# Optimization experiments

Hardware: AMD Instinct MI355X
Metric: run time of the kernel (lower is better)

## Reference

```python
import jax, jax.numpy as jnp
import numpy as np

B, N, DK, DV = 16, 4096, 64, 64


def setup_inputs() -> dict:
    key = jax.random.key(0)
    kq, kk, kv = jax.random.split(key, 3)
    q = jax.random.normal(kq, (B, N, DK), dtype=jnp.float32)
    k = jax.random.normal(kk, (B, N, DK), dtype=jnp.float32)
    v = jax.random.normal(kv, (B, N, DV), dtype=jnp.float32)
    # causal mask: positions j<=i are attendable (mask==True)
    mask = jnp.tril(jnp.ones((N, N), dtype=bool))[None, :, :]  # (1, N, N)
    return {"q": q, "k": k, "v": v, "mask": mask}


def reference(q, k, v, mask):
    # scores: (B, N, N)
    scale = 1.0 / jnp.sqrt(jnp.asarray(q.shape[-1], dtype=q.dtype))
    scores = jnp.einsum('bnd,bmd->bnm', q, k) * scale
    scores = jnp.where(mask, scores, jnp.asarray(-jnp.inf, dtype=scores.dtype))
    attn = jax.nn.softmax(scores, axis=-1)
    # dropout is identity in eval/reference mode
    return jnp.einsum('bnm,bmd->bnd', attn, v)
```

## Files before the change

### kernel.cpp

```cpp
#include <hip/hip_runtime.h>


#define N_SEQ 4096
#define DIM   64

typedef __bf16  bf16x8 __attribute__((ext_vector_type(8)));
typedef unsigned short u16x8 __attribute__((ext_vector_type(8)));
typedef float   f32x4  __attribute__((ext_vector_type(4)));
typedef short   short4v __attribute__((ext_vector_type(4)));

static __device__ __forceinline__ unsigned short f2bf(float f) {
    unsigned int u = __float_as_uint(f);
    u += 0x7FFFu + ((u >> 16) & 1u);
    return (unsigned short)(u >> 16);
}

static __device__ __forceinline__ unsigned int pk2bf(float a, float b) {
#if defined(__HIP_DEVICE_COMPILE__) && __has_builtin(__builtin_amdgcn_cvt_pk_bf16_f32)
    typedef __bf16 bf16x2_t __attribute__((ext_vector_type(2)));
    bf16x2_t r = __builtin_amdgcn_cvt_pk_bf16_f32(a, b);
    return __builtin_bit_cast(unsigned int, r);
#else
    return (unsigned int)f2bf(a) | ((unsigned int)f2bf(b) << 16);
#endif
}

static __device__ __forceinline__ float fexp2(float x) {
#if defined(__HIP_DEVICE_COMPILE__) && __has_builtin(__builtin_amdgcn_exp2f)
    return __builtin_amdgcn_exp2f(x);
#else
    return exp2f(x);
#endif
}

static __device__ __forceinline__ bf16x8 ld_frag(const void* p) {
    u16x8 u = *reinterpret_cast<const u16x8*>(p);
    return __builtin_bit_cast(bf16x8, u);
}

static __device__ __forceinline__ f32x4 mfma_pv(uint2 a, uint2 b, f32x4 c) {
#if defined(__HIP_DEVICE_COMPILE__)
#if __has_builtin(__builtin_amdgcn_mfma_f32_16x16x16bf16_1k)
    return __builtin_amdgcn_mfma_f32_16x16x16bf16_1k(
        __builtin_bit_cast(short4v, a), __builtin_bit_cast(short4v, b), c, 0, 0, 0);
#else
    f32x4 d;
    asm volatile("v_mfma_f32_16x16x16_bf16 %0, %1, %2, %3"
                 : "=v"(d) : "v"(a), "v"(b), "v"(c));
    return d;
#endif
#else
    (void)a; (void)b;
    return c;
#endif
}

static __device__ __forceinline__ void gl_lds16(const unsigned short* g, unsigned short* l) {
#if defined(__HIP_DEVICE_COMPILE__)
    __builtin_amdgcn_global_load_lds(
        (const __attribute__((address_space(1))) unsigned int*)(g),
        (__attribute__((address_space(3))) unsigned int*)(l), 16, 0, 0);
#else
    (void)g; (void)l;
#endif
}

__global__ __launch_bounds__(256)
void prep_kv(const float* __restrict__ K, const float* __restrict__ V,
             unsigned short* __restrict__ wsK, unsigned short* __restrict__ wsV) {
    const int b = blockIdx.y, t = blockIdx.x;
    if (blockIdx.z == 0) {
        const float* src = K + ((size_t)b * N_SEQ + t * 64) * DIM;
        unsigned short* dst = wsK + ((size_t)(b * 64 + t)) * 4096;
        #pragma unroll
        for (int ph = 0; ph < 2; ++ph) {
            const int gidx = threadIdx.x + ph * 256;
            const int r = gidx >> 3, g = gidx & 7;
            const float* p = src + r * DIM + g * 8;
            f32x4 f0 = *reinterpret_cast<const f32x4*>(p);
            f32x4 f1 = *reinterpret_cast<const f32x4*>(p + 4);
            uint4 w;
            w.x = pk2bf(f0[0], f0[1]); w.y = pk2bf(f0[2], f0[3]);
            w.z = pk2bf(f1[0], f1[1]); w.w = pk2bf(f1[2], f1[3]);
            *reinterpret_cast<uint4*>(&dst[(r * 8 + (g ^ (r & 7))) * 8]) = w;
        }
    } else {
        const int dv = threadIdx.x & 63;
        const int g0 = threadIdx.x >> 6;
        const float* src = V + ((size_t)b * N_SEQ + t * 64) * DIM + dv;
        unsigned short* dst = wsV + ((size_t)(b * 64 + t)) * 4096;
        #pragma unroll
        for (int ph = 0; ph < 2; ++ph) {
            const int g = g0 + ph * 4;
            float p[8];
            #pragma unroll
            for (int i = 0; i < 8; ++i)
                p[i] = src[(size_t)(g * 8 + i) * DIM];
            uint4 w;
            w.x = pk2bf(p[0], p[1]); w.y = pk2bf(p[2], p[3]);
            w.z = pk2bf(p[4], p[5]); w.w = pk2bf(p[6], p[7]);
            *reinterpret_cast<uint4*>(&dst[(dv * 8 + (g ^ (dv & 7))) * 8]) = w;
        }
    }
}

__global__ __launch_bounds__(256)
void attn_fwd(const float* __restrict__ Q, const unsigned short* __restrict__ wsK,
              const unsigned short* __restrict__ wsV, float* __restrict__ O) {
    __shared__ unsigned short kbuf[2][4096];
    __shared__ unsigned short vbuf[2][4096];

    const int tid  = threadIdx.x;
    const int wave = tid >> 6;
    const int lane = tid & 63;
    const int quad = lane >> 4;
    const int ln   = lane & 15;
    const int ln7  = lane & 7;

    const int L = (int)blockIdx.x;
    const int u = L & 255, v = L >> 8;
    const int p_ = u + ((v >> 1) << 8);
    const int b    = p_ >> 5;
    const int j    = p_ & 31;
    const int tile = (v & 1) ? (63 - j) : j;
    const int i0   = tile * 64;
    const int tmax = tile;

    const float QS = 0.125f * 1.44269504f;
    const int qrow = i0 + wave * 16 + ln;
    const float* qptr = Q + ((size_t)b * N_SEQ + qrow) * DIM;
    u16x8 qa[2];
    #pragma unroll
    for (int s = 0; s < 2; ++s) {
        const float* p = qptr + s * 32 + quad * 8;
        f32x4 f0 = *reinterpret_cast<const f32x4*>(p);
        f32x4 f1 = *reinterpret_cast<const f32x4*>(p + 4);
        #pragma unroll
        for (int jj = 0; jj < 4; ++jj) {
            qa[s][jj]     = f2bf(f0[jj] * QS);
            qa[s][4 + jj] = f2bf(f1[jj] * QS);
        }
    }

    int kaddr[8];
    #pragma unroll
    for (int s = 0; s < 2; ++s)
        #pragma unroll
        for (int nt = 0; nt < 4; ++nt)
            kaddr[s * 4 + nt] = (nt * 16 + ln) * 128 + (((s * 4 + quad) ^ ln7) * 16);
    int vaddr[16];
    #pragma unroll
    for (int nt = 0; nt < 4; ++nt)
        #pragma unroll
        for (int dvt = 0; dvt < 4; ++dvt)
            vaddr[nt * 4 + dvt] = (dvt * 16 + ln) * 128
                                + (((nt * 2 + (quad >> 1)) ^ ln7) * 16) + (quad & 1) * 8;

    const unsigned short* kt_src = wsK + (size_t)b * 64 * 4096;
    const unsigned short* vt_src = wsV + (size_t)b * 64 * 4096;
    const int dma_off = wave * 1024 + lane * 8;

    auto dma = [&](int t, int bufi) {
        const unsigned short* ks = kt_src + (size_t)t * 4096 + dma_off;
        const unsigned short* vs = vt_src + (size_t)t * 4096 + dma_off;
        #pragma unroll
        for (int i = 0; i < 2; ++i) {
            gl_lds16(ks + i * 512, &kbuf[bufi][wave * 1024 + i * 512]);
            gl_lds16(vs + i * 512, &vbuf[bufi][wave * 1024 + i * 512]);
        }
    };

    f32x4 o_acc[4] = {};
    float lsum = 0.f;

    auto compute = [&](int t, const unsigned short* kb, const unsigned short* vb) {
        f32x4 st[4] = {};
        #pragma unroll
        for (int s = 0; s < 2; ++s) {
            bf16x8 qf = __builtin_bit_cast(bf16x8, qa[s]);
            #pragma unroll
            for (int nt = 0; nt < 4; ++nt) {
                bf16x8 kf = ld_frag((const char*)kb + kaddr[s * 4 + nt]);
                st[nt] = __builtin_amdgcn_mfma_f32_16x16x32_bf16(kf, qf, st[nt], 0, 0, 0);
            }
        }
        uint2 bvv[16];
        #pragma unroll
        for (int i = 0; i < 16; ++i)
            bvv[i] = *reinterpret_cast<const uint2*>((const char*)vb + vaddr[i]);

        uint2 pk_d[4];
        if (t == tmax) {
            const int qloc = wave * 16 + ln;
            #pragma unroll
            for (int nt = 0; nt < 4; ++nt) {
                float p[4];
                #pragma unroll
                for (int r = 0; r < 4; ++r) {
                    const int kp = nt * 16 + quad * 4 + r;
                    const float x = (kp > qloc) ? -3.0e38f : st[nt][r];
                    p[r] = fexp2(x);
                    lsum += p[r];
                }
                pk_d[nt].x = pk2bf(p[0], p[1]);
                pk_d[nt].y = pk2bf(p[2], p[3]);
            }
        } else {
            #pragma unroll
            for (int nt = 0; nt < 4; ++nt) {
                float p[4];
                #pragma unroll
                for (int r = 0; r < 4; ++r) {
                    p[r] = fexp2(st[nt][r]);
                    lsum += p[r];
                }
                pk_d[nt].x = pk2bf(p[0], p[1]);
                pk_d[nt].y = pk2bf(p[2], p[3]);
            }
        }
        #pragma unroll
        for (int nt = 0; nt < 4; ++nt)
            #pragma unroll
            for (int dvt = 0; dvt < 4; ++dvt)
                o_acc[dvt] = mfma_pv(pk_d[nt], bvv[nt * 4 + dvt], o_acc[dvt]);
    };

    dma(0, 0);
    int t = 0;
    while (true) {
        __syncthreads();
        if (t < tmax) dma(t + 1, 1);
        compute(t, kbuf[0], vbuf[0]);
        if (t == tmax) break;
        ++t;
        __syncthreads();
        if (t < tmax) dma(t + 1, 0);
        compute(t, kbuf[1], vbuf[1]);
        if (t == tmax) break;
        ++t;
    }

    float s = lsum;
    s += __shfl_xor(s, 16, 64);
    s += __shfl_xor(s, 32, 64);
    float linv[4];
    #pragma unroll
    for (int r = 0; r < 4; ++r)
        linv[r] = 1.0f / __shfl(s, quad * 4 + r, 64);

    float* obase = O + ((size_t)b * N_SEQ + i0 + wave * 16) * DIM;
    #pragma unroll
    for (int r = 0; r < 4; ++r)
        #pragma unroll
        for (int dvt = 0; dvt < 4; ++dvt)
            obase[(quad * 4 + r) * DIM + dvt * 16 + ln] = o_acc[dvt][r] * linv[r];
}

extern "C" void kernel_launch(void* const* d_in, const int* in_sizes, int n_in,
                              void* d_out, int out_size, void* d_ws, size_t ws_size,
                              hipStream_t stream) {
    const float* q = (const float*)d_in[0];
    const float* k = (const float*)d_in[1];
    const float* v = (const float*)d_in[2];
    float* out = (float*)d_out;

    unsigned short* wsK = (unsigned short*)d_ws;
    unsigned short* wsV = wsK + (size_t)16 * 64 * 4096;

    prep_kv<<<dim3(64, 16, 2), dim3(256), 0, stream>>>(k, v, wsK, wsV);
    attn_fwd<<<dim3(1024), dim3(256), 0, stream>>>(q, wsK, wsV, out);
}
```

Measured before the change: 212.3 us.

## Use persistent blocks with atomic work queue and MFMA row-sum

Replaces the static 1024-block causal tile mapping with 512 persistent blocks that pull query tiles, longest first, from per-XCD atomic counters. The counters are reset in prep_kv. The goal is better load balance across the uneven causal workloads. The softmax denominator is now accumulated by an extra MFMA against a vector of ones, replacing per-lane scalar sums and shuffles. This adds an atomic plus two barriers per work item, and relies on blockIdx&7 mapping to an XCD for locality.

```diff
diff --git a/kernel.cpp b/kernel.cpp
--- a/kernel.cpp
+++ b/kernel.cpp
@@ -8,6 +8,8 @@
 typedef unsigned short u16x8 __attribute__((ext_vector_type(8)));
 typedef float   f32x4  __attribute__((ext_vector_type(4)));
 typedef short   short4v __attribute__((ext_vector_type(4)));
+
+__device__ int g_qcount[8];
 
 static __device__ __forceinline__ unsigned short f2bf(float f) {
     unsigned int u = __float_as_uint(f);
@@ -68,6 +70,8 @@
 __global__ __launch_bounds__(256)
 void prep_kv(const float* __restrict__ K, const float* __restrict__ V,
              unsigned short* __restrict__ wsK, unsigned short* __restrict__ wsV) {
+    if (blockIdx.x == 0 && blockIdx.y == 0 && blockIdx.z == 0 && threadIdx.x < 8)
+        g_qcount[threadIdx.x] = 0;
     const int b = blockIdx.y, t = blockIdx.x;
     if (blockIdx.z == 0) {
         const float* src = K + ((size_t)b * N_SEQ + t * 64) * DIM;
@@ -109,6 +113,7 @@
               const unsigned short* __restrict__ wsV, float* __restrict__ O) {
     __shared__ unsigned short kbuf[2][4096];
     __shared__ unsigned short vbuf[2][4096];
+    __shared__ int s_item;
 
     const int tid  = threadIdx.x;
     const int wave = tid >> 6;
@@ -116,31 +121,7 @@
     const int quad = lane >> 4;
     const int ln   = lane & 15;
     const int ln7  = lane & 7;
-
-    const int L = (int)blockIdx.x;
-    const int u = L & 255, v = L >> 8;
-    const int p_ = u + ((v >> 1) << 8);
-    const int b    = p_ >> 5;
-    const int j    = p_ & 31;
-    const int tile = (v & 1) ? (63 - j) : j;
-    const int i0   = tile * 64;
-    const int tmax = tile;
-
-    const float QS = 0.125f * 1.44269504f;
-    const int qrow = i0 + wave * 16 + ln;
-    const float* qptr = Q + ((size_t)b * N_SEQ + qrow) * DIM;
-    u16x8 qa[2];
-    #pragma unroll
-    for (int s = 0; s < 2; ++s) {
-        const float* p = qptr + s * 32 + quad * 8;
-        f32x4 f0 = *reinterpret_cast<const f32x4*>(p);
-        f32x4 f1 = *reinterpret_cast<const f32x4*>(p + 4);
-        #pragma unroll
-        for (int jj = 0; jj < 4; ++jj) {
-            qa[s][jj]     = f2bf(f0[jj] * QS);
-            qa[s][4 + jj] = f2bf(f1[jj] * QS);
-        }
-    }
+    const int r    = (int)blockIdx.x & 7;
 
     int kaddr[8];
     #pragma unroll
@@ -156,104 +137,120 @@
             vaddr[nt * 4 + dvt] = (dvt * 16 + ln) * 128
                                 + (((nt * 2 + (quad >> 1)) ^ ln7) * 16) + (quad & 1) * 8;
 
-    const unsigned short* kt_src = wsK + (size_t)b * 64 * 4096;
-    const unsigned short* vt_src = wsV + (size_t)b * 64 * 4096;
     const int dma_off = wave * 1024 + lane * 8;
-
-    auto dma = [&](int t, int bufi) {
-        const unsigned short* ks = kt_src + (size_t)t * 4096 + dma_off;
-        const unsigned short* vs = vt_src + (size_t)t * 4096 + dma_off;
-        #pragma unroll
-        for (int i = 0; i < 2; ++i) {
-            gl_lds16(ks + i * 512, &kbuf[bufi][wave * 1024 + i * 512]);
-            gl_lds16(vs + i * 512, &vbuf[bufi][wave * 1024 + i * 512]);
-        }
-    };
-
-    f32x4 o_acc[4] = {};
-    float lsum = 0.f;
-
-    auto compute = [&](int t, const unsigned short* kb, const unsigned short* vb) {
-        f32x4 st[4] = {};
+    const uint2 ones  = make_uint2(0x3F803F80u, 0x3F803F80u);
+    const float QS = 0.125f * 1.44269504f;
+
+    for (;;) {
+        __syncthreads();
+        if (tid == 0) s_item = atomicAdd(&g_qcount[r], 1);
+        __syncthreads();
+        const int item = s_item;
+        if (item >= 128) break;
+
+        const int tile = 63 - (item >> 1);
+        const int b    = r * 2 + (item & 1);
+        const int i0   = tile * 64;
+        const int tmax = tile;
+
+        const float* qptr = Q + ((size_t)b * N_SEQ + i0 + wave * 16 + ln) * DIM;
+        u16x8 qa[2];
         #pragma unroll
         for (int s = 0; s < 2; ++s) {
-            bf16x8 qf = __builtin_bit_cast(bf16x8, qa[s]);
+            const float* p = qptr + s * 32 + quad * 8;
+            f32x4 f0 = *reinterpret_cast<const f32x4*>(p);
+            f32x4 f1 = *reinterpret_cast<const f32x4*>(p + 4);
+            #pragma unroll
+            for (int jj = 0; jj < 4; ++jj) {
+                qa[s][jj]     = f2bf(f0[jj] * QS);
+                qa[s][4 + jj] = f2bf(f1[jj] * QS);
+            }
+        }
+
+        const unsigned short* kt_src = wsK + (size_t)b * 64 * 4096;
+        const unsigned short* vt_src = wsV + (size_t)b * 64 * 4096;
+
+        auto dma = [&](int t, int bufi) {
+            const unsigned short* ks = kt_src + (size_t)t * 4096 + dma_off;
+            const unsigned short* vs = vt_src + (size_t)t * 4096 + dma_off;
+            #pragma unroll
+            for (int i = 0; i < 2; ++i) {
+                gl_lds16(ks + i * 512, &kbuf[bufi][wave * 1024 + i * 512]);
+                gl_lds16(vs + i * 512, &vbuf[bufi][wave * 1024 + i * 512]);
+            }
+        };
+
+        f32x4 o_acc[4] = {};
+        f32x4 lacc = {};
+
+        auto compute = [&](int t, const unsigned short* kb, const unsigned short* vb) {
+            f32x4 st[4] = {};
+            #pragma unroll
+            for (int s = 0; s < 2; ++s) {
+                bf16x8 qf = __builtin_bit_cast(bf16x8, qa[s]);
+                #pragma unroll
+                for (int nt = 0; nt < 4; ++nt) {
+                    bf16x8 kf = ld_frag((const char*)kb + kaddr[s * 4 + nt]);
+                    st[nt] = __builtin_amdgcn_mfma_f32_16x16x32_bf16(kf, qf, st[nt], 0, 0, 0);
+                }
+            }
+            uint2 bvv[16];
+            #pragma unroll
+            for (int i = 0; i < 16; ++i)
+                bvv[i] = *reinterpret_cast<const uint2*>((const char*)vb + vaddr[i]);
+
+            uint2 pk_d[4];
+            if (t == tmax) {
+                const int qloc = wave * 16 + ln;
+                #pragma unroll
+                for (int nt = 0; nt < 4; ++nt) {
+                    float p0 = fexp2((nt * 16 + quad * 4 + 0 > qloc) ? -3.0e38f : st[nt][0]);
+                    float p1 = fexp2((nt * 16 + quad * 4 + 1 > qloc) ? -3.0e38f : st[nt][1]);
+                    float p2 = fexp2((nt * 16 + quad * 4 + 2 > qloc) ? -3.0e38f : st[nt][2]);
+                    float p3 = fexp2((nt * 16 + quad * 4 + 3 > qloc) ? -3.0e38f : st[nt][3]);
+                    pk_d[nt].x = pk2bf(p0, p1);
+                    pk_d[nt].y = pk2bf(p2, p3);
+                }
+            } else {
+                #pragma unroll
+                for (int nt = 0; nt < 4; ++nt) {
+                    pk_d[nt].x = pk2bf(fexp2(st[nt][0]), fexp2(st[nt][1]));
+                    pk_d[nt].y = pk2bf(fexp2(st[nt][2]), fexp2(st[nt][3]));
+                }
+            }
             #pragma unroll
             for (int nt = 0; nt < 4; ++nt) {
-                bf16x8 kf = ld_frag((const char*)kb + kaddr[s * 4 + nt]);
-                st[nt] = __builtin_amdgcn_mfma_f32_16x16x32_bf16(kf, qf, st[nt], 0, 0, 0);
-            }
-        }
-        uint2 bvv[16];
-        #pragma unroll
-        for (int i = 0; i < 16; ++i)
-            bvv[i] = *reinterpret_cast<const uint2*>((const char*)vb + vaddr[i]);
-
-        uint2 pk_d[4];
-        if (t == tmax) {
-            const int qloc = wave * 16 + ln;
-            #pragma unroll
-            for (int nt = 0; nt < 4; ++nt) {
-                float p[4];
-                #pragma unroll
-                for (int r = 0; r < 4; ++r) {
-                    const int kp = nt * 16 + quad * 4 + r;
-                    const float x = (kp > qloc) ? -3.0e38f : st[nt][r];
-                    p[r] = fexp2(x);
-                    lsum += p[r];
-                }
-                pk_d[nt].x = pk2bf(p[0], p[1]);
-                pk_d[nt].y = pk2bf(p[2], p[3]);
-            }
-        } else {
-            #pragma unroll
-            for (int nt = 0; nt < 4; ++nt) {
-                float p[4];
-                #pragma unroll
-                for (int r = 0; r < 4; ++r) {
-                    p[r] = fexp2(st[nt][r]);
-                    lsum += p[r];
-                }
-                pk_d[nt].x = pk2bf(p[0], p[1]);
-                pk_d[nt].y = pk2bf(p[2], p[3]);
-            }
-        }
-        #pragma unroll
-        for (int nt = 0; nt < 4; ++nt)
+                #pragma unroll
+                for (int dvt = 0; dvt < 4; ++dvt)
+                    o_acc[dvt] = mfma_pv(pk_d[nt], bvv[nt * 4 + dvt], o_acc[dvt]);
+                lacc = mfma_pv(pk_d[nt], ones, lacc);
+            }
+        };
+
+        dma(0, 0);
+        int t = 0;
+        while (true) {
+            __syncthreads();
+            if (t < tmax) dma(t + 1, 1);
+            compute(t, kbuf[0], vbuf[0]);
+            if (t == tmax) break;
+            ++t;
+            __syncthreads();
+            if (t < tmax) dma(t + 1, 0);
+            compute(t, kbuf[1], vbuf[1]);
+            if (t == tmax) break;
+            ++t;
+        }
+
+        float* obase = O + ((size_t)b * N_SEQ + i0 + wave * 16) * DIM;
+        #pragma unroll
+        for (int rr = 0; rr < 4; ++rr) {
+            const float inv = 1.0f / lacc[rr];
             #pragma unroll
             for (int dvt = 0; dvt < 4; ++dvt)
-                o_acc[dvt] = mfma_pv(pk_d[nt], bvv[nt * 4 + dvt], o_acc[dvt]);
-    };
-
-    dma(0, 0);
-    int t = 0;
-    while (true) {
-        __syncthreads();
-        if (t < tmax) dma(t + 1, 1);
-        compute(t, kbuf[0], vbuf[0]);
-        if (t == tmax) break;
-        ++t;
-        __syncthreads();
-        if (t < tmax) dma(t + 1, 0);
-        compute(t, kbuf[1], vbuf[1]);
-        if (t == tmax) break;
-        ++t;
+                obase[(quad * 4 + rr) * DIM + dvt * 16 + ln] = o_acc[dvt][rr] * inv;
+        }
     }
-
-    float s = lsum;
-    s += __shfl_xor(s, 16, 64);
-    s += __shfl_xor(s, 32, 64);
-    float linv[4];
-    #pragma unroll
-    for (int r = 0; r < 4; ++r)
-        linv[r] = 1.0f / __shfl(s, quad * 4 + r, 64);
-
-    float* obase = O + ((size_t)b * N_SEQ + i0 + wave * 16) * DIM;
-    #pragma unroll
-    for (int r = 0; r < 4; ++r)
-        #pragma unroll
-        for (int dvt = 0; dvt < 4; ++dvt)
-            obase[(quad * 4 + r) * DIM + dvt * 16 + ln] = o_acc[dvt][r] * linv[r];
 }
 
 extern "C" void kernel_launch(void* const* d_in, const int* in_sizes, int n_in,
@@ -268,5 +265,5 @@
     unsigned short* wsV = wsK + (size_t)16 * 64 * 4096;
 
     prep_kv<<<dim3(64, 16, 2), dim3(256), 0, stream>>>(k, v, wsK, wsV);
-    attn_fwd<<<dim3(1024), dim3(256), 0, stream>>>(q, wsK, wsV, out);
-}
+    attn_fwd<<<dim3(512), dim3(256), 0, stream>>>(q, wsK, wsV, out);
+}
```

After: 202.8 us. 1.05x faster.
